# Optimization experiments

Hardware: AMD Instinct MI355X
Metric: run time of the kernel (lower is better)

The kernel has to match this reference:

```python
import jax, jax.numpy as jnp
import numpy as np


def setup_inputs() -> dict:
    key = jax.random.key(0)
    k1, k2 = jax.random.split(key)
    B, C, H, W = 4, 256, 64, 64
    f_m = jax.random.normal(k1, (B, C, H, W), dtype=jnp.float32)
    f_d = jax.random.normal(k2, (B, C, H, W), dtype=jnp.float32)
    return {"f_m": f_m, "f_d": f_d}


def reference(f_m, f_d):
    B, C, H, W = f_d.shape
    HW = H * W
    f_fuse = f_m + f_d                      # [B, C, H, W]
    f_c = f_fuse.reshape(B, C, HW)          # [B, C, HW]
    # scores[b, n, m] = sum_c f_c[b, c, n] * f_c[b, c, m]
    scores = jnp.einsum('bcn,bcm->bnm', f_c, f_c)   # [B, HW, HW]
    att = jax.nn.softmax(scores, axis=-1)           # softmax over last dim
    f_d_r = f_d.reshape(B, C, HW)                   # [B, C, HW]
    # out[b, c, m] = sum_n f_d_r[b, c, n] * att[b, n, m]
    f_d_att = jnp.einsum('bcn,bnm->bcm', f_d_r, att).reshape(B, C, H, W)
    return f_d_att + f_d
```

## Files before the change

kernel.cpp:

```cpp
#include <hip/hip_runtime.h>
#include <math.h>

#define B_ 4
#define C_ 256
#define N_ 4096
#define LDE 68
#define LDX 72

typedef __attribute__((ext_vector_type(8))) short short8;
typedef __attribute__((ext_vector_type(4))) float f32x4;
typedef __attribute__((ext_vector_type(2))) float f32x2;

__device__ inline ushort f2bf(float f) {
    uint u = __float_as_uint(f);
    return (ushort)((u + 0x7fffu + ((u >> 16) & 1u)) >> 16);
}
__device__ inline float bf2f(ushort h) { return __uint_as_float(((uint)h) << 16); }

__device__ inline f32x4 mfma16(short8 a, short8 b, f32x4 c) {
    return __builtin_amdgcn_mfma_f32_16x16x32_bf16(a, b, c, 0, 0, 0);
}
__device__ inline f32x4 mfma8(long a, long b, f32x4 c) {
    return __builtin_amdgcn_mfma_f32_16x16x32_fp8_fp8(a, b, c, 0, 0, 0);
}

__device__ inline size_t xfi8(int b, int nt, int kk) {
    return (((size_t)(b * 256 + nt)) * 8 + kk) * 512;
}
__device__ inline size_t ffi(int b, int nc, int ct, int k2) {
    return ((((size_t)(b * 64 + nc)) * 16 + ct) * 2 + k2) * 512;
}
__device__ inline size_t eti(int b, int mt, int ng) {
    return (((size_t)(b * 256 + mt)) * 512 + (size_t)ng) * 128;
}
__device__ inline size_t zmi(int b, int nc, int mt) {
    return ((size_t)(b * 64 + nc)) * 256 + mt;
}

__global__ __launch_bounds__(256) void prep_x_kernel(const float* __restrict__ fm,
                                                     const float* __restrict__ fd,
                                                     uchar* __restrict__ xfrag8) {
    __shared__ ushort xl[64][LDX];
    const int b = blockIdx.z, c0 = blockIdx.y * 64, n0 = blockIdx.x * 64;
    const int t = threadIdx.x;
    const int n4 = (t & 15) * 4, cl = t >> 4;
    const size_t base = (size_t)b * C_ * N_;
    #pragma unroll
    for (int p = 0; p < 4; ++p) {
        const int cr = 16 * p + cl;
        const float4 m4 = *(const float4*)(fm + base + (size_t)(c0 + cr) * N_ + n0 + n4);
        const float4 d4 = *(const float4*)(fd + base + (size_t)(c0 + cr) * N_ + n0 + n4);
        ushort4 xo;
        xo.x = f2bf(m4.x + d4.x); xo.y = f2bf(m4.y + d4.y);
        xo.z = f2bf(m4.z + d4.z); xo.w = f2bf(m4.w + d4.w);
        *(ushort4*)(&xl[cr][n4]) = xo;
    }
    __syncthreads();
    const int l = t & 63, tl = t >> 6;
    const int nl = 16 * tl + (l & 15);
    #pragma unroll
    for (int j = 0; j < 2; ++j) {
        const int kk = (c0 >> 5) + j;
        const int cb = 32 * j + 8 * (l >> 4);
        float f[8];
        #pragma unroll
        for (int i = 0; i < 8; ++i) f[i] = bf2f(xl[cb + i][nl]);
        int d0 = __builtin_amdgcn_cvt_pk_fp8_f32(f[0], f[1], 0, 0);
        d0 = __builtin_amdgcn_cvt_pk_fp8_f32(f[2], f[3], d0, 1);
        int d1 = __builtin_amdgcn_cvt_pk_fp8_f32(f[4], f[5], 0, 0);
        d1 = __builtin_amdgcn_cvt_pk_fp8_f32(f[6], f[7], d1, 1);
        uint* dst = (uint*)(xfrag8 + xfi8(b, (n0 >> 4) + tl, kk) + (size_t)l * 8);
        dst[0] = (uint)d0; dst[1] = (uint)d1;
    }
}

__global__ __launch_bounds__(256) void dg_kernel(const uchar* __restrict__ xfrag8,
                                                 float* __restrict__ dgall,
                                                 float* __restrict__ rsadd) {
    const int t = threadIdx.x, lane = t & 63, w = t >> 6;
    const int tid = blockIdx.x * 4 + w;
    const int b = tid >> 8, nt = tid & 255;
    const int l15 = lane & 15, q = lane >> 4;
    long af[8];
    #pragma unroll
    for (int kk = 0; kk < 8; ++kk)
        af[kk] = *(const long*)(xfrag8 + xfi8(b, nt, kk) + (size_t)lane * 8);
    f32x4 dacc = {0.f, 0.f, 0.f, 0.f};
    #pragma unroll
    for (int kk = 0; kk < 8; ++kk)
        dacc = mfma8(af[kk], af[kk], dacc);
    float dvv[4];
    #pragma unroll
    for (int r = 0; r < 4; ++r)
        dvv[r] = __shfl(dacc[r], 20 * q + r, 64);
    if (l15 == 0) {
        #pragma unroll
        for (int r = 0; r < 4; ++r)
            dgall[b * N_ + 16 * nt + 4 * q + r] = dvv[r];
    }
    const int zi = blockIdx.x * 256 + t;
    if (zi < B_ * N_) rsadd[zi] = 0.f;
}

__global__ __launch_bounds__(512, 2) void lsum_t_kernel(const uchar* __restrict__ xfrag8,
                                                        const float* __restrict__ dgall,
                                                        uchar* __restrict__ E8,
                                                        uchar* __restrict__ zmask,
                                                        float* __restrict__ rsbase,
                                                        float* __restrict__ rsadd) {
    __shared__ float red[8][64];
    __shared__ uchar chl[34];
    __shared__ int cnt_s;
    __shared__ uint zst[34];
    const int bid = blockIdx.x;
    const int b = (bid >> 1) & 3;
    const int n0 = ((((bid >> 3) << 1) | (bid & 1))) * 64;
    const int j = n0 >> 6;
    const int t = threadIdx.x, lane = t & 63, w = t >> 6;
    const int l15 = lane & 15, q = lane >> 4;
    const int g = w >> 2, wm = w & 3;

    if (t == 0) {
        int c = 0;
        chl[c++] = (uchar)j;
        for (int k = 0; k < 64; ++k) {
            if (k == j) continue;
            const bool own = (k > j) ? (((j + k) & 1) == 0) : (((j + k) & 1) == 1);
            if (own) chl[c++] = (uchar)k;
        }
        cnt_s = c;
    }
    if (t < 34) zst[t] = 0u;

    long af[4][8];
    #pragma unroll
    for (int ns = 0; ns < 4; ++ns)
        #pragma unroll
        for (int kk = 0; kk < 8; ++kk)
            af[ns][kk] = *(const long*)(xfrag8 + xfi8(b, (n0 >> 4) + ns, kk) + (size_t)lane * 8);

    float dv[4][4];
    #pragma unroll
    for (int ns = 0; ns < 4; ++ns)
        #pragma unroll
        for (int r = 0; r < 4; ++r)
            dv[ns][r] = dgall[b * N_ + n0 + 16 * ns + 4 * q + r];

    __syncthreads();
    const int cnt = cnt_s;

    long bn[8];
    float dgm_cur;
    {
        const int mt0 = 4 * (int)chl[g] + wm;
        #pragma unroll
        for (int kk = 0; kk < 8; ++kk)
            bn[kk] = *(const long*)(xfrag8 + xfi8(b, mt0, kk) + (size_t)lane * 8);
        dgm_cur = dgall[b * N_ + 16 * mt0 + l15];
    }
    const size_t ebl = (size_t)l15 * 8 + 4 * (q & 1);
    const int ngb = (n0 >> 3) + (q >> 1);

    float rs[4][4] = {};
    for (int it = 0; it < 17; ++it) {
        const int idx = 2 * it + g;
        const bool valid = idx < cnt;
        const int kc = chl[valid ? idx : 0];
        const int mt = 4 * kc + wm;
        int idxn = 2 * (it + 1) + g; if (idxn >= cnt) idxn = 0;
        const int mtn = 4 * (int)chl[idxn] + wm;

        f32x4 a0 = {0.f,0.f,0.f,0.f}, a1 = {0.f,0.f,0.f,0.f};
        f32x4 a2 = {0.f,0.f,0.f,0.f}, a3 = {0.f,0.f,0.f,0.f};
        __builtin_amdgcn_s_setprio(1);
        #pragma unroll
        for (int kk = 0; kk < 8; ++kk) {
            const long bc = bn[kk];
            a0 = mfma8(af[0][kk], bc, a0);
            a1 = mfma8(af[1][kk], bc, a1);
            a2 = mfma8(af[2][kk], bc, a2);
            a3 = mfma8(af[3][kk], bc, a3);
            bn[kk] = *(const long*)(xfrag8 + xfi8(b, mtn, kk) + (size_t)lane * 8);
        }
        __builtin_amdgcn_s_setprio(0);
        const float dgm = dgm_cur;
        dgm_cur = dgall[b * N_ + 16 * mtn + l15];

        float df[4][4];
#define EDF(AA, NS)                                                    \
        df[NS][0] = AA[0] - dv[NS][0]; df[NS][1] = AA[1] - dv[NS][1];  \
        df[NS][2] = AA[2] - dv[NS][2]; df[NS][3] = AA[3] - dv[NS][3];
        EDF(a0, 0) EDF(a1, 1) EDF(a2, 2) EDF(a3, 3)
#undef EDF
        const float mxA = fmaxf(
            fmaxf(fmaxf(fmaxf(df[0][0], df[0][1]), fmaxf(df[0][2], df[0][3])),
                  fmaxf(fmaxf(df[1][0], df[1][1]), fmaxf(df[1][2], df[1][3]))),
            fmaxf(fmaxf(fmaxf(df[2][0], df[2][1]), fmaxf(df[2][2], df[2][3])),
                  fmaxf(fmaxf(df[3][0], df[3][1]), fmaxf(df[3][2], df[3][3]))));
        const bool nzA = valid && (__ballot(mxA > -30.0f) != 0ULL);
        if (valid && lane == 0) zmask[zmi(b, j, mt)] = nzA ? 1 : 0;
        if (nzA) {
            uint dpk[4];
#define EEXP(NS)                                                                       \
            {                                                                          \
                float e0 = __expf(df[NS][0]), e1 = __expf(df[NS][1]);                  \
                float e2 = __expf(df[NS][2]), e3 = __expf(df[NS][3]);                  \
                rs[NS][0] += e0; rs[NS][1] += e1; rs[NS][2] += e2; rs[NS][3] += e3;    \
                int d = __builtin_amdgcn_cvt_pk_fp8_f32(e0, e1, 0, 0);                 \
                d = __builtin_amdgcn_cvt_pk_fp8_f32(e2, e3, d, 1);                     \
                dpk[NS] = (uint)d;                                                     \
            }
            EEXP(0) EEXP(1) EEXP(2) EEXP(3)
#undef EEXP
            #pragma unroll
            for (int ns = 0; ns < 4; ++ns)
                *(uint*)(E8 + eti(b, mt, ngb + 2 * ns) + ebl) = dpk[ns];
        }
        if (valid && kc != j) {
            float dfB[4][4];
            #pragma unroll
            for (int ns = 0; ns < 4; ++ns) {
                dfB[ns][0] = (ns==0?a0[0]:ns==1?a1[0]:ns==2?a2[0]:a3[0]) - dgm;
                dfB[ns][1] = (ns==0?a0[1]:ns==1?a1[1]:ns==2?a2[1]:a3[1]) - dgm;
                dfB[ns][2] = (ns==0?a0[2]:ns==1?a1[2]:ns==2?a2[2]:a3[2]) - dgm;
                dfB[ns][3] = (ns==0?a0[3]:ns==1?a1[3]:ns==2?a2[3]:a3[3]) - dgm;
            }
            uint bits = 0;
            #pragma unroll
            for (int ns = 0; ns < 4; ++ns) {
                const float m2 = fmaxf(fmaxf(dfB[ns][0], dfB[ns][1]),
                                       fmaxf(dfB[ns][2], dfB[ns][3]));
                if (__ballot(m2 > -30.0f) != 0ULL) bits |= (1u << ns);
            }
            if (bits) {
                if (lane == 0) atomicOr(&zst[idx], bits);
                float cs = 0.f;
                #pragma unroll
                for (int ns = 0; ns < 4; ++ns)
                    #pragma unroll
                    for (int r = 0; r < 4; ++r)
                        cs += __expf(dfB[ns][r]);
                cs += __shfl_xor(cs, 16, 64);
                cs += __shfl_xor(cs, 32, 64);
                if (q == 0) atomicAdd(rsadd + b * N_ + 16 * mt + l15, cs);
            }
        }
    }
    #pragma unroll
    for (int off = 1; off < 16; off <<= 1)
        #pragma unroll
        for (int ns = 0; ns < 4; ++ns)
            #pragma unroll
            for (int r = 0; r < 4; ++r)
                rs[ns][r] += __shfl_xor(rs[ns][r], off, 64);
    if (l15 == 0) {
        #pragma unroll
        for (int ns = 0; ns < 4; ++ns)
            #pragma unroll
            for (int r = 0; r < 4; ++r)
                red[w][16 * ns + 4 * q + r] = rs[ns][r];
    }
    __syncthreads();
    if (t < 64) {
        float s = 0.f;
        #pragma unroll
        for (int ww = 0; ww < 8; ++ww) s += red[ww][t];
        rsbase[b * N_ + n0 + t] = s;
    }
    if (t >= 64 && t < 64 + 33 * 4) {
        const int ii = (t - 64) >> 2, ns = (t - 64) & 3;
        const int idx = ii + 1;
        if (idx < cnt) {
            const int kc = chl[idx];
            zmask[zmi(b, kc, 4 * j + ns)] = (((zst[idx] >> ns) & 1u) != 0u) ? 2 : 0;
        }
    }
}

__global__ __launch_bounds__(512, 2) void out_e_kernel(const uchar* __restrict__ E8,
                                                       const uchar* __restrict__ zmask,
                                                       const float* __restrict__ rsbase,
                                                       const float* __restrict__ rsadd,
                                                       const float* __restrict__ dgall,
                                                       const uchar* __restrict__ xfrag8,
                                                       const float* __restrict__ fd32,
                                                       float* __restrict__ outp) {
    __shared__ ushort esc[8][16][66];
    const int bid = blockIdx.x;
    const int b = (bid >> 1) & 3;
    const int m0 = ((((bid >> 3) << 1) | (bid & 1))) * 64;
    const int t = threadIdx.x, lane = t & 63, w = t >> 6;
    const int l15 = lane & 15, q = lane >> 4;
    const size_t fb = (size_t)b * C_ * N_;
    const uchar* mrow = zmask + zmi(b, 0, m0 >> 4);

    f32x4 acc[2][4];
    #pragma unroll
    for (int ct = 0; ct < 2; ++ct)
        #pragma unroll
        for (int mt = 0; mt < 4; ++mt)
            acc[ct][mt] = (f32x4){0.f, 0.f, 0.f, 0.f};

    for (int gg = 0; gg < 8; ++gg) {
        uint mk[8];
        #pragma unroll
        for (int i = 0; i < 8; ++i)
            mk[i] = *(const uint*)(mrow + (size_t)(8 * gg + i) * 256);
        #pragma unroll
        for (int i = 0; i < 8; ++i) {
            const uint mki = mk[i];
            if (mki == 0) continue;
            const int nc = 8 * gg + i;
            const float* rb = rsbase + b * N_ + 64 * nc + 8 * q;
            const float* ra = rsadd + b * N_ + 64 * nc + 8 * q;
            float4 s0[2], s1[2];
            #pragma unroll
            for (int k2 = 0; k2 < 2; ++k2) {
                const float4 b0 = *(const float4*)(rb + 32 * k2);
                const float4 b1 = *(const float4*)(rb + 32 * k2 + 4);
                const float4 a0v = *(const float4*)(ra + 32 * k2);
                const float4 a1v = *(const float4*)(ra + 32 * k2 + 4);
                s0[k2].x = 1.0f / (b0.x + a0v.x); s0[k2].y = 1.0f / (b0.y + a0v.y);
                s0[k2].z = 1.0f / (b0.z + a0v.z); s0[k2].w = 1.0f / (b0.w + a0v.w);
                s1[k2].x = 1.0f / (b1.x + a1v.x); s1[k2].y = 1.0f / (b1.y + a1v.y);
                s1[k2].z = 1.0f / (b1.z + a1v.z); s1[k2].w = 1.0f / (b1.w + a1v.w);
            }
            short8 fn[2][2];
            #pragma unroll
            for (int ct = 0; ct < 2; ++ct) {
                const int c = 32 * w + 16 * ct + l15;
                const float* frow = fd32 + fb + (size_t)c * N_ + 64 * nc + 8 * q;
                #pragma unroll
                for (int k2 = 0; k2 < 2; ++k2) {
                    const float4 fa = *(const float4*)(frow + 32 * k2);
                    const float4 fb4 = *(const float4*)(frow + 32 * k2 + 4);
                    union { ushort us[8]; short8 v; } u;
                    u.us[0] = f2bf(fa.x * s0[k2].x); u.us[1] = f2bf(fa.y * s0[k2].y);
                    u.us[2] = f2bf(fa.z * s0[k2].z); u.us[3] = f2bf(fa.w * s0[k2].w);
                    u.us[4] = f2bf(fb4.x * s1[k2].x); u.us[5] = f2bf(fb4.y * s1[k2].y);
                    u.us[6] = f2bf(fb4.z * s1[k2].z); u.us[7] = f2bf(fb4.w * s1[k2].w);
                    fn[ct][k2] = u.v;
                }
            }
            if ((mki & ~0x01010101u) == 0u) {
                #pragma unroll
                for (int k2 = 0; k2 < 2; ++k2) {
                    #pragma unroll
                    for (int mt = 0; mt < 4; ++mt) {
                        if (((mki >> (8 * mt)) & 0xffu) != 1u) continue;
                        const long e8 = *(const long*)(E8 + eti(b, (m0 >> 4) + mt, 8 * nc + 4 * k2 + q) + (size_t)l15 * 8);
                        const uint lo = (uint)(unsigned long)e8;
                        const uint hi = (uint)((unsigned long)e8 >> 32);
                        const f32x2 f01 = __builtin_amdgcn_cvt_pk_f32_fp8((int)lo, false);
                        const f32x2 f23 = __builtin_amdgcn_cvt_pk_f32_fp8((int)lo, true);
                        const f32x2 f45 = __builtin_amdgcn_cvt_pk_f32_fp8((int)hi, false);
                        const f32x2 f67 = __builtin_amdgcn_cvt_pk_f32_fp8((int)hi, true);
                        union { uint u[4]; short8 v; } be;
                        asm("v_cvt_pk_bf16_f32 %0, %1, %2" : "=v"(be.u[0]) : "v"(f01.x), "v"(f01.y));
                        asm("v_cvt_pk_bf16_f32 %0, %1, %2" : "=v"(be.u[1]) : "v"(f23.x), "v"(f23.y));
                        asm("v_cvt_pk_bf16_f32 %0, %1, %2" : "=v"(be.u[2]) : "v"(f45.x), "v"(f45.y));
                        asm("v_cvt_pk_bf16_f32 %0, %1, %2" : "=v"(be.u[3]) : "v"(f67.x), "v"(f67.y));
                        acc[0][mt] = mfma16(fn[0][k2], be.v, acc[0][mt]);
                        acc[1][mt] = mfma16(fn[1][k2], be.v, acc[1][mt]);
                    }
                }
            } else {
                #pragma unroll
                for (int mt = 0; mt < 4; ++mt) {
                    long bmf[8];
                    #pragma unroll
                    for (int kk = 0; kk < 8; ++kk)
                        bmf[kk] = *(const long*)(xfrag8 + xfi8(b, (m0 >> 4) + mt, kk) + (size_t)lane * 8);
                    #pragma unroll
                    for (int nt = 0; nt < 4; ++nt) {
                        long anf[8];
                        #pragma unroll
                        for (int kk = 0; kk < 8; ++kk)
                            anf[kk] = *(const long*)(xfrag8 + xfi8(b, 4 * nc + nt, kk) + (size_t)lane * 8);
                        f32x4 sacc = {0.f, 0.f, 0.f, 0.f};
                        #pragma unroll
                        for (int kk = 0; kk < 8; ++kk)
                            sacc = mfma8(anf[kk], bmf[kk], sacc);
                        #pragma unroll
                        for (int r = 0; r < 4; ++r) {
                            const float gv = dgall[b * N_ + 64 * nc + 16 * nt + 4 * q + r];
                            esc[w][l15][16 * nt + 4 * q + r] = f2bf(__expf(sacc[r] - gv));
                        }
                    }
                    #pragma unroll
                    for (int k2 = 0; k2 < 2; ++k2) {
                        const short8 be = *(const short8*)(&esc[w][l15][32 * k2 + 8 * q]);
                        acc[0][mt] = mfma16(fn[0][k2], be, acc[0][mt]);
                        acc[1][mt] = mfma16(fn[1][k2], be, acc[1][mt]);
                    }
                }
            }
        }
    }
    #pragma unroll
    for (int ct = 0; ct < 2; ++ct)
        #pragma unroll
        for (int mt = 0; mt < 4; ++mt)
            #pragma unroll
            for (int r = 0; r < 4; ++r) {
                const int c = 32 * w + 16 * ct + 4 * q + r;
                const int m = m0 + 16 * mt + l15;
                const size_t o = fb + (size_t)c * N_ + m;
                outp[o] = acc[ct][mt][r] + fd32[o];
            }
}

__global__ __launch_bounds__(256) void prep_kernel(const float* __restrict__ fm,
                                                   const float* __restrict__ fd,
                                                   uchar* __restrict__ xfrag8,
                                                   ushort* __restrict__ ffrag) {
    __shared__ ushort xl[64][LDX];
    __shared__ ushort fl[64][LDX];
    const int b = blockIdx.z, c0 = blockIdx.y * 64, n0 = blockIdx.x * 64;
    const int t = threadIdx.x;
    const int n4 = (t & 15) * 4, cl = t >> 4;
    const size_t base = (size_t)b * C_ * N_;
    #pragma unroll
    for (int p = 0; p < 4; ++p) {
        const int cr = 16 * p + cl;
        const float4 m4 = *(const float4*)(fm + base + (size_t)(c0 + cr) * N_ + n0 + n4);
        const float4 d4 = *(const float4*)(fd + base + (size_t)(c0 + cr) * N_ + n0 + n4);
        ushort4 fo;
        fo.x = f2bf(d4.x); fo.y = f2bf(d4.y); fo.z = f2bf(d4.z); fo.w = f2bf(d4.w);
        *(ushort4*)(&fl[cr][n4]) = fo;
        ushort4 xo;
        xo.x = f2bf(m4.x + d4.x); xo.y = f2bf(m4.y + d4.y);
        xo.z = f2bf(m4.z + d4.z); xo.w = f2bf(m4.w + d4.w);
        *(ushort4*)(&xl[cr][n4]) = xo;
    }
    __syncthreads();
    const int l = t & 63, tl = t >> 6;
    {
        const int nl = 16 * tl + (l & 15);
        #pragma unroll
        for (int j = 0; j < 2; ++j) {
            const int kk = (c0 >> 5) + j;
            const int cb = 32 * j + 8 * (l >> 4);
            float f[8];
            #pragma unroll
            for (int i = 0; i < 8; ++i) f[i] = bf2f(xl[cb + i][nl]);
            int d0 = __builtin_amdgcn_cvt_pk_fp8_f32(f[0], f[1], 0, 0);
            d0 = __builtin_amdgcn_cvt_pk_fp8_f32(f[2], f[3], d0, 1);
            int d1 = __builtin_amdgcn_cvt_pk_fp8_f32(f[4], f[5], 0, 0);
            d1 = __builtin_amdgcn_cvt_pk_fp8_f32(f[6], f[7], d1, 1);
            uint* dst = (uint*)(xfrag8 + xfi8(b, (n0 >> 4) + tl, kk) + (size_t)l * 8);
            dst[0] = (uint)d0; dst[1] = (uint)d1;
        }
    }
    {
        const int row = 16 * tl + (l & 15);
        #pragma unroll
        for (int k2 = 0; k2 < 2; ++k2) {
            const int col = 32 * k2 + 8 * (l >> 4);
            const ushort4 a0 = *(const ushort4*)(&fl[row][col]);
            const ushort4 a1 = *(const ushort4*)(&fl[row][col + 4]);
            ushort* dst = ffrag + ffi(b, n0 >> 6, (c0 >> 4) + tl, k2) + l * 8;
            *(ushort4*)(dst) = a0; *(ushort4*)(dst + 4) = a1;
        }
    }
}

__global__ __launch_bounds__(512, 2) void lsum_g_kernel(const uchar* __restrict__ xfrag8,
                                                        float* __restrict__ lg) {
    __shared__ float red[8][64];
    __shared__ float dgl[64];
    const int bid = blockIdx.x;
    const int b = (bid >> 1) & 3;
    const int n0 = ((((bid >> 3) << 1) | (bid & 1))) * 64;
    const int t = threadIdx.x, lane = t & 63, w = t >> 6;
    const int l15 = lane & 15, q = lane >> 4;

    long af[4][8];
    #pragma unroll
    for (int ns = 0; ns < 4; ++ns)
        #pragma unroll
        for (int kk = 0; kk < 8; ++kk)
            af[ns][kk] = *(const long*)(xfrag8 + xfi8(b, (n0 >> 4) + ns, kk) + (size_t)lane * 8);

    float dv[4][4];
    #pragma unroll
    for (int ns = 0; ns < 4; ++ns) {
        f32x4 dacc = {0.f, 0.f, 0.f, 0.f};
        #pragma unroll
        for (int kk = 0; kk < 8; ++kk)
            dacc = mfma8(af[ns][kk], af[ns][kk], dacc);
        #pragma unroll
        for (int r = 0; r < 4; ++r)
            dv[ns][r] = __shfl(dacc[r], 20 * q + r, 64);
    }
    if (w == 0 && l15 == 0) {
        #pragma unroll
        for (int ns = 0; ns < 4; ++ns)
            #pragma unroll
            for (int r = 0; r < 4; ++r)
                dgl[16 * ns + 4 * q + r] = dv[ns][r];
    }

    long bn[8];
    #pragma unroll
    for (int kk = 0; kk < 8; ++kk)
        bn[kk] = *(const long*)(xfrag8 + xfi8(b, w, kk) + (size_t)lane * 8);

    float rs[4][4] = {};
    for (int mc = 0; mc < 32; ++mc) {
        const int mtn = (mc + 1 < 32) ? (mc + 1) * 8 + w : w;
        f32x4 a0 = {0.f,0.f,0.f,0.f}, a1 = {0.f,0.f,0.f,0.f};
        f32x4 a2 = {0.f,0.f,0.f,0.f}, a3 = {0.f,0.f,0.f,0.f};
        #pragma unroll
        for (int kk = 0; kk < 8; ++kk) {
            const long bc = bn[kk];
            a0 = mfma8(af[0][kk], bc, a0);
            a1 = mfma8(af[1][kk], bc, a1);
            a2 = mfma8(af[2][kk], bc, a2);
            a3 = mfma8(af[3][kk], bc, a3);
            bn[kk] = *(const long*)(xfrag8 + xfi8(b, mtn, kk) + (size_t)lane * 8);
        }
        #pragma unroll
        for (int r = 0; r < 4; ++r) {
            rs[0][r] += __expf(a0[r] - dv[0][r]);
            rs[1][r] += __expf(a1[r] - dv[1][r]);
            rs[2][r] += __expf(a2[r] - dv[2][r]);
            rs[3][r] += __expf(a3[r] - dv[3][r]);
        }
    }
    #pragma unroll
    for (int off = 1; off < 16; off <<= 1)
        #pragma unroll
        for (int ns = 0; ns < 4; ++ns)
            #pragma unroll
            for (int r = 0; r < 4; ++r)
                rs[ns][r] += __shfl_xor(rs[ns][r], off, 64);
    if (l15 == 0) {
        #pragma unroll
        for (int ns = 0; ns < 4; ++ns)
            #pragma unroll
            for (int r = 0; r < 4; ++r)
                red[w][16 * ns + 4 * q + r] = rs[ns][r];
    }
    __syncthreads();
    if (t < 64) {
        float s = 0.f;
        #pragma unroll
        for (int ww = 0; ww < 8; ++ww) s += red[ww][t];
        lg[b * N_ + n0 + t] = dgl[t] + __logf(s);
    }
}

__global__ __launch_bounds__(512, 2) void out_g_kernel(const uchar* __restrict__ xfrag8,
                                                       const ushort* __restrict__ ffrag,
                                                       const float* __restrict__ gg,
                                                       const float* __restrict__ fd32,
                                                       float* __restrict__ outp) {
    __shared__ ushort ET[2][64][LDE];
    const int bid = blockIdx.x;
    const int b = (bid >> 1) & 3;
    const int m0 = ((((bid >> 3) << 1) | (bid & 1))) * 64;
    const int t = threadIdx.x, lane = t & 63, w = t >> 6;
    const int l15 = lane & 15, q = lane >> 4;
    const int a = w & 3, h = w >> 2;
    const size_t fb = (size_t)b * C_ * N_;

    long bfr[2][8];
    #pragma unroll
    for (int jt = 0; jt < 2; ++jt)
        #pragma unroll
        for (int kk = 0; kk < 8; ++kk)
            bfr[jt][kk] = *(const long*)(xfrag8 + xfi8(b, (m0 >> 4) + 2 * h + jt, kk) + (size_t)lane * 8);

    f32x4 acc[2][4];
    #pragma unroll
    for (int ct = 0; ct < 2; ++ct)
        #pragma unroll
        for (int mt = 0; mt < 4; ++mt)
            acc[ct][mt] = (f32x4){0.f, 0.f, 0.f, 0.f};

    long an[8];
    #pragma unroll
    for (int kk = 0; kk < 8; ++kk)
        an[kk] = *(const long*)(xfrag8 + xfi8(b, a, kk) + (size_t)lane * 8);
    float gn[4];
    #pragma unroll
    for (int r = 0; r < 4; ++r) gn[r] = gg[b * N_ + 16 * a + 4 * q + r];

    int p = 0;
    for (int n0c = 0; n0c < N_; n0c += 64, p ^= 1) {
        const int nc = n0c >> 6;
        short8 fn[2][2];
        #pragma unroll
        for (int ct = 0; ct < 2; ++ct)
            #pragma unroll
            for (int k2 = 0; k2 < 2; ++k2)
                fn[ct][k2] = *(const short8*)(ffrag + ffi(b, nc, 2 * w + ct, k2) + lane * 8);
        float gv[4];
        #pragma unroll
        for (int r = 0; r < 4; ++r) gv[r] = gn[r];
        const int nx = (n0c + 64 < N_) ? n0c + 64 : 0;
        #pragma unroll
        for (int r = 0; r < 4; ++r) gn[r] = gg[b * N_ + nx + 16 * a + 4 * q + r];

        f32x4 s0 = {0.f, 0.f, 0.f, 0.f}, s1 = {0.f, 0.f, 0.f, 0.f};
        #pragma unroll
        for (int kk = 0; kk < 8; ++kk) {
            s0 = mfma8(an[kk], bfr[0][kk], s0);
            s1 = mfma8(an[kk], bfr[1][kk], s1);
            an[kk] = *(const long*)(xfrag8 + xfi8(b, (nx >> 4) + a, kk) + (size_t)lane * 8);
        }
        ushort4 e0, e1;
        e0.x = f2bf(__expf(s0[0] - gv[0])); e0.y = f2bf(__expf(s0[1] - gv[1]));
        e0.z = f2bf(__expf(s0[2] - gv[2])); e0.w = f2bf(__expf(s0[3] - gv[3]));
        e1.x = f2bf(__expf(s1[0] - gv[0])); e1.y = f2bf(__expf(s1[1] - gv[1]));
        e1.z = f2bf(__expf(s1[2] - gv[2])); e1.w = f2bf(__expf(s1[3] - gv[3]));
        *(ushort4*)(&ET[p][32 * h + l15][16 * a + 4 * q])      = e0;
        *(ushort4*)(&ET[p][32 * h + 16 + l15][16 * a + 4 * q]) = e1;

        asm volatile("s_waitcnt lgkmcnt(0)\n\ts_barrier" ::: "memory");

        #pragma unroll
        for (int k2 = 0; k2 < 2; ++k2) {
            #pragma unroll
            for (int mt = 0; mt < 4; ++mt) {
                const short8 be = *(const short8*)(&ET[p][16 * mt + l15][32 * k2 + 8 * q]);
                acc[0][mt] = mfma16(fn[0][k2], be, acc[0][mt]);
                acc[1][mt] = mfma16(fn[1][k2], be, acc[1][mt]);
            }
        }
    }
    #pragma unroll
    for (int ct = 0; ct < 2; ++ct)
        #pragma unroll
        for (int mt = 0; mt < 4; ++mt)
            #pragma unroll
            for (int r = 0; r < 4; ++r) {
                const int c = 32 * w + 16 * ct + 4 * q + r;
                const int m = m0 + 16 * mt + l15;
                const size_t o = fb + (size_t)c * N_ + m;
                outp[o] = acc[ct][mt][r] + fd32[o];
            }
}

extern "C" void kernel_launch(void* const* d_in, const int* in_sizes, int n_in,
                              void* d_out, int out_size, void* d_ws, size_t ws_size,
                              hipStream_t stream) {
    const float* fm = (const float*)d_in[0];
    const float* fd = (const float*)d_in[1];
    float* outp = (float*)d_out;

    const size_t xb_elts = (size_t)B_ * N_ * C_;
    const size_t e_bytes = (size_t)B_ * N_ * N_;
    const size_t z_bytes = (size_t)B_ * 64 * 256;
    const size_t f_bytes = (size_t)B_ * N_ * 4;
    const size_t need_e  = xb_elts + e_bytes + z_bytes + 3 * f_bytes;
    const size_t need_g  = xb_elts * 3 + f_bytes;

    uchar* xfrag8 = (uchar*)d_ws;

    if (ws_size >= need_e) {
        uchar* E8     = xfrag8 + xb_elts;
        uchar* zmask  = E8 + e_bytes;
        float* rsbase = (float*)(zmask + z_bytes);
        float* rsadd  = rsbase + (size_t)B_ * N_;
        float* dgall  = rsadd + (size_t)B_ * N_;
        prep_x_kernel<<<dim3(N_ / 64, C_ / 64, B_), 256, 0, stream>>>(fm, fd, xfrag8);
        dg_kernel<<<dim3(256), 256, 0, stream>>>(xfrag8, dgall, rsadd);
        lsum_t_kernel<<<dim3(256), 512, 0, stream>>>(xfrag8, dgall, E8, zmask, rsbase, rsadd);
        out_e_kernel<<<dim3(256), 512, 0, stream>>>(E8, zmask, rsbase, rsadd, dgall, xfrag8, fd, outp);
    } else if (ws_size >= need_g) {
        ushort* ffrag = (ushort*)(xfrag8 + xb_elts);
        float*  lg    = (float*)(xfrag8 + xb_elts * 3);
        prep_kernel<<<dim3(N_ / 64, C_ / 64, B_), 256, 0, stream>>>(fm, fd, xfrag8, ffrag);
        lsum_g_kernel<<<dim3(256), 512, 0, stream>>>(xfrag8, lg);
        out_g_kernel<<<dim3(256), 512, 0, stream>>>(xfrag8, ffrag, lg, fd, outp);
    }
}
```

Before: 111.2 us.

## Widen fp8 fragment layout to 16-byte loads and skip cold tiles early

The fp8 fragment layout is changed so that each lane holds two consecutive k-chunks contiguously. The prep, dg, lsum and out kernels can then use 16-byte vector loads instead of 8-byte ones. In lsum_t the kernel now computes a cheap upper bound (max score minus min diagonal) and skips the whole exp/pack/transpose path for tiles where every entry would underflow. zmask is pre-zeroed in dg_kernel so only non-zero flags need writing. The risk is that the bound check adds a reduction and ballot per iteration, and skipped tiles rely on the pre-zeroed mask being correct.

```diff
diff --git a/kernel.cpp b/kernel.cpp
--- a/kernel.cpp
+++ b/kernel.cpp
@@ -10,6 +10,7 @@
 typedef __attribute__((ext_vector_type(8))) short short8;
 typedef __attribute__((ext_vector_type(4))) float f32x4;
 typedef __attribute__((ext_vector_type(2))) float f32x2;
+typedef __attribute__((ext_vector_type(2))) long long2v;
 
 __device__ inline ushort f2bf(float f) {
     uint u = __float_as_uint(f);
@@ -24,6 +25,9 @@
     return __builtin_amdgcn_mfma_f32_16x16x32_fp8_fp8(a, b, c, 0, 0, 0);
 }
 
+__device__ inline size_t xfi16(int b, int nt, int kk2) {
+    return (((size_t)(b * 256 + nt)) * 4 + kk2) * 1024;
+}
 __device__ inline size_t xfi8(int b, int nt, int kk) {
     return (((size_t)(b * 256 + nt)) * 8 + kk) * 512;
 }
@@ -58,9 +62,9 @@
     __syncthreads();
     const int l = t & 63, tl = t >> 6;
     const int nl = 16 * tl + (l & 15);
+    uint dd[4];
     #pragma unroll
     for (int j = 0; j < 2; ++j) {
-        const int kk = (c0 >> 5) + j;
         const int cb = 32 * j + 8 * (l >> 4);
         float f[8];
         #pragma unroll
@@ -69,26 +73,30 @@
         d0 = __builtin_amdgcn_cvt_pk_fp8_f32(f[2], f[3], d0, 1);
         int d1 = __builtin_amdgcn_cvt_pk_fp8_f32(f[4], f[5], 0, 0);
         d1 = __builtin_amdgcn_cvt_pk_fp8_f32(f[6], f[7], d1, 1);
-        uint* dst = (uint*)(xfrag8 + xfi8(b, (n0 >> 4) + tl, kk) + (size_t)l * 8);
-        dst[0] = (uint)d0; dst[1] = (uint)d1;
-    }
+        dd[2 * j] = (uint)d0; dd[2 * j + 1] = (uint)d1;
+    }
+    uint* dst = (uint*)(xfrag8 + xfi16(b, (n0 >> 4) + tl, c0 >> 6) + (size_t)l * 16);
+    dst[0] = dd[0]; dst[1] = dd[1]; dst[2] = dd[2]; dst[3] = dd[3];
 }
 
 __global__ __launch_bounds__(256) void dg_kernel(const uchar* __restrict__ xfrag8,
                                                  float* __restrict__ dgall,
-                                                 float* __restrict__ rsadd) {
+                                                 float* __restrict__ rsadd,
+                                                 uchar* __restrict__ zmask) {
     const int t = threadIdx.x, lane = t & 63, w = t >> 6;
     const int tid = blockIdx.x * 4 + w;
     const int b = tid >> 8, nt = tid & 255;
     const int l15 = lane & 15, q = lane >> 4;
-    long af[8];
-    #pragma unroll
-    for (int kk = 0; kk < 8; ++kk)
-        af[kk] = *(const long*)(xfrag8 + xfi8(b, nt, kk) + (size_t)lane * 8);
+    long2v af[4];
+    #pragma unroll
+    for (int kk2 = 0; kk2 < 4; ++kk2)
+        af[kk2] = *(const long2v*)(xfrag8 + xfi16(b, nt, kk2) + (size_t)lane * 16);
     f32x4 dacc = {0.f, 0.f, 0.f, 0.f};
     #pragma unroll
-    for (int kk = 0; kk < 8; ++kk)
-        dacc = mfma8(af[kk], af[kk], dacc);
+    for (int kk2 = 0; kk2 < 4; ++kk2) {
+        dacc = mfma8(af[kk2].x, af[kk2].x, dacc);
+        dacc = mfma8(af[kk2].y, af[kk2].y, dacc);
+    }
     float dvv[4];
     #pragma unroll
     for (int r = 0; r < 4; ++r)
@@ -100,6 +108,7 @@
     }
     const int zi = blockIdx.x * 256 + t;
     if (zi < B_ * N_) rsadd[zi] = 0.f;
+    zmask[zi] = 0;
 }
 
 __global__ __launch_bounds__(512, 2) void lsum_t_kernel(const uchar* __restrict__ xfrag8,
@@ -132,12 +141,12 @@
     }
     if (t < 34) zst[t] = 0u;
 
-    long af[4][8];
+    long2v af[4][4];
     #pragma unroll
     for (int ns = 0; ns < 4; ++ns)
         #pragma unroll
-        for (int kk = 0; kk < 8; ++kk)
-            af[ns][kk] = *(const long*)(xfrag8 + xfi8(b, (n0 >> 4) + ns, kk) + (size_t)lane * 8);
+        for (int kk2 = 0; kk2 < 4; ++kk2)
+            af[ns][kk2] = *(const long2v*)(xfrag8 + xfi16(b, (n0 >> 4) + ns, kk2) + (size_t)lane * 16);
 
     float dv[4][4];
     #pragma unroll
@@ -145,17 +154,23 @@
         #pragma unroll
         for (int r = 0; r < 4; ++r)
             dv[ns][r] = dgall[b * N_ + n0 + 16 * ns + 4 * q + r];
+    float dvmin = dv[0][0];
+    #pragma unroll
+    for (int ns = 0; ns < 4; ++ns)
+        #pragma unroll
+        for (int r = 0; r < 4; ++r)
+            dvmin = fminf(dvmin, dv[ns][r]);
 
     __syncthreads();
     const int cnt = cnt_s;
 
-    long bn[8];
+    long2v bn[4];
     float dgm_cur;
     {
         const int mt0 = 4 * (int)chl[g] + wm;
         #pragma unroll
-        for (int kk = 0; kk < 8; ++kk)
-            bn[kk] = *(const long*)(xfrag8 + xfi8(b, mt0, kk) + (size_t)lane * 8);
+        for (int kk2 = 0; kk2 < 4; ++kk2)
+            bn[kk2] = *(const long2v*)(xfrag8 + xfi16(b, mt0, kk2) + (size_t)lane * 16);
         dgm_cur = dgall[b * N_ + 16 * mt0 + l15];
     }
     const size_t ebl = (size_t)l15 * 8 + 4 * (q & 1);
@@ -174,17 +189,29 @@
         f32x4 a2 = {0.f,0.f,0.f,0.f}, a3 = {0.f,0.f,0.f,0.f};
         __builtin_amdgcn_s_setprio(1);
         #pragma unroll
-        for (int kk = 0; kk < 8; ++kk) {
-            const long bc = bn[kk];
-            a0 = mfma8(af[0][kk], bc, a0);
-            a1 = mfma8(af[1][kk], bc, a1);
-            a2 = mfma8(af[2][kk], bc, a2);
-            a3 = mfma8(af[3][kk], bc, a3);
-            bn[kk] = *(const long*)(xfrag8 + xfi8(b, mtn, kk) + (size_t)lane * 8);
+        for (int kk2 = 0; kk2 < 4; ++kk2) {
+            const long2v bc = bn[kk2];
+            a0 = mfma8(af[0][kk2].x, bc.x, a0);
+            a1 = mfma8(af[1][kk2].x, bc.x, a1);
+            a2 = mfma8(af[2][kk2].x, bc.x, a2);
+            a3 = mfma8(af[3][kk2].x, bc.x, a3);
+            a0 = mfma8(af[0][kk2].y, bc.y, a0);
+            a1 = mfma8(af[1][kk2].y, bc.y, a1);
+            a2 = mfma8(af[2][kk2].y, bc.y, a2);
+            a3 = mfma8(af[3][kk2].y, bc.y, a3);
+            bn[kk2] = *(const long2v*)(xfrag8 + xfi16(b, mtn, kk2) + (size_t)lane * 16);
         }
         __builtin_amdgcn_s_setprio(0);
         const float dgm = dgm_cur;
         dgm_cur = dgall[b * N_ + 16 * mtn + l15];
+
+        const float gmax = fmaxf(
+            fmaxf(fmaxf(fmaxf(a0[0], a0[1]), fmaxf(a0[2], a0[3])),
+                  fmaxf(fmaxf(a1[0], a1[1]), fmaxf(a1[2], a1[3]))),
+            fmaxf(fmaxf(fmaxf(a2[0], a2[1]), fmaxf(a2[2], a2[3])),
+                  fmaxf(fmaxf(a3[0], a3[1]), fmaxf(a3[2], a3[3]))));
+        const bool hot = valid && (__ballot(gmax - fminf(dvmin, dgm) > -30.0f) != 0ULL);
+        if (!hot) continue;
 
         float df[4][4];
 #define EDF(AA, NS)                                                    \
@@ -197,9 +224,9 @@
                   fmaxf(fmaxf(df[1][0], df[1][1]), fmaxf(df[1][2], df[1][3]))),
             fmaxf(fmaxf(fmaxf(df[2][0], df[2][1]), fmaxf(df[2][2], df[2][3])),
                   fmaxf(fmaxf(df[3][0], df[3][1]), fmaxf(df[3][2], df[3][3]))));
-        const bool nzA = valid && (__ballot(mxA > -30.0f) != 0ULL);
-        if (valid && lane == 0) zmask[zmi(b, j, mt)] = nzA ? 1 : 0;
+        const bool nzA = (__ballot(mxA > -30.0f) != 0ULL);
         if (nzA) {
+            if (lane == 0) zmask[zmi(b, j, mt)] = 1;
             uint dpk[4];
 #define EEXP(NS)                                                                       \
             {                                                                          \
@@ -216,7 +243,7 @@
             for (int ns = 0; ns < 4; ++ns)
                 *(uint*)(E8 + eti(b, mt, ngb + 2 * ns) + ebl) = dpk[ns];
         }
-        if (valid && kc != j) {
+        if (kc != j) {
             float dfB[4][4];
             #pragma unroll
             for (int ns = 0; ns < 4; ++ns) {
@@ -272,7 +299,7 @@
         const int idx = ii + 1;
         if (idx < cnt) {
             const int kc = chl[idx];
-            zmask[zmi(b, kc, 4 * j + ns)] = (((zst[idx] >> ns) & 1u) != 0u) ? 2 : 0;
+            if ((zst[idx] >> ns) & 1u) zmask[zmi(b, kc, 4 * j + ns)] = 2;
         }
     }
 }
@@ -367,20 +394,22 @@
             } else {
                 #pragma unroll
                 for (int mt = 0; mt < 4; ++mt) {
-                    long bmf[8];
+                    long2v bmf[4];
                     #pragma unroll
-                    for (int kk = 0; kk < 8; ++kk)
-                        bmf[kk] = *(const long*)(xfrag8 + xfi8(b, (m0 >> 4) + mt, kk) + (size_t)lane * 8);
+                    for (int kk2 = 0; kk2 < 4; ++kk2)
+                        bmf[kk2] = *(const long2v*)(xfrag8 + xfi16(b, (m0 >> 4) + mt, kk2) + (size_t)lane * 16);
                     #pragma unroll
                     for (int nt = 0; nt < 4; ++nt) {
-                        long anf[8];
+                        long2v anf[4];
                         #pragma unroll
-                        for (int kk = 0; kk < 8; ++kk)
-                            anf[kk] = *(const long*)(xfrag8 + xfi8(b, 4 * nc + nt, kk) + (size_t)lane * 8);
+                        for (int kk2 = 0; kk2 < 4; ++kk2)
+                            anf[kk2] = *(const long2v*)(xfrag8 + xfi16(b, 4 * nc + nt, kk2) + (size_t)lane * 16);
                         f32x4 sacc = {0.f, 0.f, 0.f, 0.f};
                         #pragma unroll
-                        for (int kk = 0; kk < 8; ++kk)
-                            sacc = mfma8(anf[kk], bmf[kk], sacc);
+                        for (int kk2 = 0; kk2 < 4; ++kk2) {
+                            sacc = mfma8(anf[kk2].x, bmf[kk2].x, sacc);
+                            sacc = mfma8(anf[kk2].y, bmf[kk2].y, sacc);
+                        }
                         #pragma unroll
                         for (int r = 0; r < 4; ++r) {
                             const float gv = dgall[b * N_ + 64 * nc + 16 * nt + 4 * q + r];
@@ -666,7 +695,7 @@
         float* rsadd  = rsbase + (size_t)B_ * N_;
         float* dgall  = rsadd + (size_t)B_ * N_;
         prep_x_kernel<<<dim3(N_ / 64, C_ / 64, B_), 256, 0, stream>>>(fm, fd, xfrag8);
-        dg_kernel<<<dim3(256), 256, 0, stream>>>(xfrag8, dgall, rsadd);
+        dg_kernel<<<dim3(256), 256, 0, stream>>>(xfrag8, dgall, rsadd, zmask);
         lsum_t_kernel<<<dim3(256), 512, 0, stream>>>(xfrag8, dgall, E8, zmask, rsbase, rsadd);
         out_e_kernel<<<dim3(256), 512, 0, stream>>>(E8, zmask, rsbase, rsadd, dgall, xfrag8, fd, outp);
     } else if (ws_size >= need_g) {
```

Measured after the change: 109.1 us. Within noise of the previous version (-1.8%).
